# Performance work log

Measured on AMD Instinct MI355X. Metric: run time of the kernel, lower is better.

The kernel has to match this reference:

```python
import jax, jax.numpy as jnp
import numpy as np

B, T, NLAT, N, D = 8, 4, 64, 2048, 1024
HEADS, HEAD_DIM = 16, 64
ADIM = HEADS * HEAD_DIM
EPS = 1e-5


def layer_norm(x, w, b):
    mu = jnp.mean(x, axis=-1, keepdims=True)
    var = jnp.var(x, axis=-1, keepdims=True)
    return (x - mu) * jax.lax.rsqrt(var + EPS) * w + b


def setup_inputs() -> dict:
    key = jax.random.key(0)
    ks = jax.random.split(key, 8)
    s = 0.02
    return {
        "latents": jax.random.normal(ks[0], (B, T, NLAT, D), jnp.float32),
        "x": jax.random.normal(ks[1], (B, T, N, D), jnp.float32),
        "Wq": jax.random.normal(ks[2], (D, ADIM), jnp.float32) * s,     # [in, out]
        "Wkv": jax.random.normal(ks[3], (D, 2 * ADIM), jnp.float32) * s,
        "Wout": jax.random.normal(ks[4], (ADIM, D), jnp.float32) * s,
        "bout": jnp.zeros((D,), jnp.float32),
        "lnl_w": jnp.ones((D,), jnp.float32),
        "lnl_b": jnp.zeros((D,), jnp.float32),
        "lnm_w": jnp.ones((D,), jnp.float32),
        "lnm_b": jnp.zeros((D,), jnp.float32),
    }


def reference(latents, x, Wq, Wkv, Wout, bout, lnl_w, lnl_b, lnm_w, lnm_b):
    scale = HEAD_DIM ** (-0.5)
    lat = layer_norm(latents, lnl_w, lnl_b)          # [B,T,NLAT,D]
    med = layer_norm(x, lnm_w, lnm_b)                # [B,T,N,D]
    q = lat @ Wq                                      # [B,T,NLAT,ADIM]
    kv_in = jnp.concatenate((med, lat), axis=-2)      # [B,T,N+NLAT,D]
    kv = kv_in @ Wkv                                  # [B,T,N+NLAT,2*ADIM]
    k, v = jnp.split(kv, 2, axis=-1)
    # split heads: b t n (h d) -> b h t n d
    def split_heads(z):
        b, t, n, _ = z.shape
        return z.reshape(b, t, n, HEADS, HEAD_DIM).transpose(0, 3, 1, 2, 4)
    q = split_heads(q) * scale
    k = split_heads(k)
    v = split_heads(v)
    scores = jnp.einsum('bhtid,bhtjd->bhtij', q, k)   # [B,H,T,NLAT,N+NLAT]
    attn = jax.nn.softmax(scores, axis=-1)            # max-subtract handled internally
    out = jnp.einsum('bhtij,bhtjd->bhtid', attn, v)   # [B,H,T,NLAT,HEAD_DIM]
    out = out.transpose(0, 2, 3, 1, 4).reshape(B, T, NLAT, ADIM)
    return out @ Wout + bout
```

## Files before the change

kernel.cpp:

```cpp
#include <hip/hip_runtime.h>
#include <hip/hip_bf16.h>
#include <stdint.h>

#define B_    8
#define T_    4
#define NLAT  64
#define NMED  2048
#define NKV   2112
#define D_    1024
#define HEADS 16
#define HD    64
#define ADIM  1024
#define BT    32

#define GK    1024
#define GN    2048
#define GM    67584
#define NSLC  32
#define NWG_BIG 2144

typedef __attribute__((ext_vector_type(8))) short bf16x8;
typedef __attribute__((ext_vector_type(4))) float f32x4;

__device__ __forceinline__ ushort f2bf(float f) {
  union { float f; uint32_t u; } v; v.f = f;
  return (ushort)((v.u + 0x7fff + ((v.u >> 16) & 1)) >> 16);
}

__device__ __forceinline__ void gload_lds16(const void* g, void* l) {
  __builtin_amdgcn_global_load_lds(
      (const __attribute__((address_space(1))) void*)g,
      (__attribute__((address_space(3))) void*)l, 16, 0, 0);
}

__device__ __forceinline__ f32x4 mfma16(bf16x8 a, bf16x8 b, f32x4 c) {
  return __builtin_amdgcn_mfma_f32_16x16x32_bf16(a, b, c, 0, 0, 0);
}

__global__ __launch_bounds__(256) void wtrans(const float* __restrict__ src,
                                              ushort* __restrict__ dst,
                                              int K, int Nm) {
  __shared__ float t[64][65];
  const int tr = blockIdx.y, tc = blockIdx.x;
  const int c = threadIdx.x & 63;
  const int r4 = threadIdx.x >> 6;
#pragma unroll
  for (int rr = 0; rr < 16; ++rr) {
    int r = r4 + rr * 4;
    t[r][c] = src[(size_t)(tr * 64 + r) * Nm + tc * 64 + c];
  }
  __syncthreads();
#pragma unroll
  for (int rr = 0; rr < 16; ++rr) {
    int n = r4 + rr * 4;
    dst[(size_t)(tc * 64 + n) * K + tr * 64 + c] = f2bf(t[c][n]);
  }
}

__global__ __launch_bounds__(256) void ln_kernel(
    const float* __restrict__ lat, const float* __restrict__ x,
    const float* __restrict__ lnl_w, const float* __restrict__ lnl_b,
    const float* __restrict__ lnm_w, const float* __restrict__ lnm_b,
    ushort* __restrict__ kvin) {
  const int row = blockIdx.x;
  const int bt = row / NKV;
  const int j = row - bt * NKV;
  const float* src;
  const float* w;
  const float* bb;
  if (j < NMED) {
    src = x + ((size_t)bt * NMED + j) * D_;
    w = lnm_w; bb = lnm_b;
  } else {
    src = lat + ((size_t)bt * NLAT + (j - NMED)) * D_;
    w = lnl_w; bb = lnl_b;
  }
  const int tid = threadIdx.x;
  float4 v = ((const float4*)src)[tid];
  float s = v.x + v.y + v.z + v.w;
  float s2 = v.x * v.x + v.y * v.y + v.z * v.z + v.w * v.w;
#pragma unroll
  for (int off = 1; off < 64; off <<= 1) {
    s += __shfl_xor(s, off, 64);
    s2 += __shfl_xor(s2, off, 64);
  }
  __shared__ float red[8];
  const int wave = tid >> 6;
  if ((tid & 63) == 0) { red[wave] = s; red[4 + wave] = s2; }
  __syncthreads();
  float S = red[0] + red[1] + red[2] + red[3];
  float S2 = red[4] + red[5] + red[6] + red[7];
  const float inv = 1.f / (float)D_;
  float mu = S * inv;
  float var = S2 * inv - mu * mu;
  float rs = rsqrtf(var + 1e-5f);
  float4 wv = ((const float4*)w)[tid];
  float4 bv = ((const float4*)bb)[tid];
  ushort4 ov;
  ov.x = f2bf((v.x - mu) * rs * wv.x + bv.x);
  ov.y = f2bf((v.y - mu) * rs * wv.y + bv.y);
  ov.z = f2bf((v.z - mu) * rs * wv.z + bv.z);
  ov.w = f2bf((v.w - mu) * rs * wv.w + bv.w);
  ((ushort4*)(kvin + (size_t)row * D_))[tid] = ov;
}

template <int AMODE, int OUTMODE>
__global__ __launch_bounds__(256, 3) void gemm128(const ushort* __restrict__ A,
                                                  const ushort* __restrict__ Bt,
                                                  void* __restrict__ C,
                                                  const float* __restrict__ bias,
                                                  int ntx, int nwg, int K, int ldc) {
  __shared__ ushort lsA[128 * 32];
  __shared__ ushort lsB[128 * 32];
  const int tid = threadIdx.x;
  const int lane = tid & 63;
  const int wave = tid >> 6;
  const int lr = lane & 15;
  const int lg = lane >> 4;
  const int wr = (wave >> 1) * 64;
  const int wc = (wave & 1) * 64;

  const int g = blockIdx.x;
  const int cpx = nwg >> 3;
  const int v = (g & 7) * cpx + (g >> 3);
  const int bx = v % ntx;
  const int by = v / ntx;
  const long brow = (long)by * 128;
  const int bcol = bx * 128;

  const int pcx = lg ^ ((lr >> 1) & 3);

  f32x4 acc[4][4];
#pragma unroll
  for (int m = 0; m < 4; ++m)
#pragma unroll
    for (int n = 0; n < 4; ++n) acc[m][n] = (f32x4){0.f, 0.f, 0.f, 0.f};

  const int s0 = tid, s1 = 256 + tid;
  const int r0 = s0 >> 2, r1 = s1 >> 2;
  const int c0 = (s0 & 3) ^ ((s0 >> 3) & 3);
  const int c1 = (s1 & 3) ^ ((s1 >> 3) & 3);
  const int o0 = (s0 & ~63) * 16;
  const int o1 = (s1 & ~63) * 16;

  long arow0, arow1;
  if (AMODE == 1) {
    int g0 = (int)brow + r0, g1 = (int)brow + r1;
    arow0 = (long)(g0 >> 6) * NKV + NMED + (g0 & 63);
    arow1 = (long)(g1 >> 6) * NKV + NMED + (g1 & 63);
  } else {
    arow0 = brow + r0;
    arow1 = brow + r1;
  }
  const long browB0 = (long)(bcol + r0) * K;
  const long browB1 = (long)(bcol + r1) * K;

  for (int k0 = 0; k0 < K; k0 += 32) {
    gload_lds16(A + arow0 * (long)K + k0 + c0 * 8, (char*)lsA + o0);
    gload_lds16(A + arow1 * (long)K + k0 + c1 * 8, (char*)lsA + o1);
    gload_lds16(Bt + browB0 + k0 + c0 * 8, (char*)lsB + o0);
    gload_lds16(Bt + browB1 + k0 + c1 * 8, (char*)lsB + o1);
    __syncthreads();

    bf16x8 af[4], bf[4];
#pragma unroll
    for (int m = 0; m < 4; ++m)
      af[m] = *(const bf16x8*)((char*)lsA + (wr + m * 16 + lr) * 64 + pcx * 16);
#pragma unroll
    for (int n = 0; n < 4; ++n)
      bf[n] = *(const bf16x8*)((char*)lsB + (wc + n * 16 + lr) * 64 + pcx * 16);
#pragma unroll
    for (int m = 0; m < 4; ++m)
#pragma unroll
      for (int n = 0; n < 4; ++n)
        acc[m][n] = mfma16(bf[n], af[m], acc[m][n]);
    __syncthreads();
  }

#pragma unroll
  for (int m = 0; m < 4; ++m) {
    long row = brow + wr + m * 16 + lr;
#pragma unroll
    for (int n = 0; n < 4; ++n) {
      int coln = bcol + wc + n * 16 + lg * 4;
      long off = row * (long)ldc + coln;
      if (OUTMODE == 2) {
        float4 bv = *(const float4*)(bias + coln);
        float4 o;
        o.x = acc[m][n][0] + bv.x;
        o.y = acc[m][n][1] + bv.y;
        o.z = acc[m][n][2] + bv.z;
        o.w = acc[m][n][3] + bv.w;
        *(float4*)((float*)C + off) = o;
      } else {
        const float sc = (OUTMODE == 1) ? 0.125f : 1.f;
        ushort4 o;
        o.x = f2bf(acc[m][n][0] * sc);
        o.y = f2bf(acc[m][n][1] * sc);
        o.z = f2bf(acc[m][n][2] * sc);
        o.w = f2bf(acc[m][n][3] * sc);
        *(ushort4*)((ushort*)C + off) = o;
      }
    }
  }
}

__global__ __launch_bounds__(512, 2) void gemm256(const ushort* __restrict__ A,
                                                  const ushort* __restrict__ BtKV,
                                                  const ushort* __restrict__ BtQ,
                                                  ushort* __restrict__ Ckv,
                                                  ushort* __restrict__ Cq) {
  extern __shared__ __align__(16) char smem[];
  const int tid = threadIdx.x;
  const int lane = tid & 63;
  const int wv = tid >> 6;
  const int wm = wv >> 2;
  const int wn = wv & 3;
  const int lr = lane & 15;
  const int lg = lane >> 4;

  const int g = blockIdx.x;
  const int v = (g & 7) * (NWG_BIG / 8) + (g >> 3);
  const bool isq = v >= 2112;
  long brow; int bcol;
  const ushort* Bp; ushort* Cp; int ldc;
  if (!isq) {
    brow = (long)(v >> 3) * 256;
    bcol = (v & 7) * 256;
    Bp = BtKV; Cp = Ckv; ldc = GN;
  } else {
    int u = v - 2112;
    brow = (long)(u >> 2) * 256;
    bcol = (u & 3) * 256;
    Bp = BtQ; Cp = Cq; ldc = ADIM;
  }
  const float sc = isq ? 0.125f : 1.f;

  const int pcx = lg ^ ((lr >> 1) & 3);
  const int rbA = wm * 128 + lr;
  const int rbB = wn * 64 + lr;

  f32x4 acc[8][4];
#pragma unroll
  for (int m = 0; m < 8; ++m)
#pragma unroll
    for (int n = 0; n < 4; ++n) acc[m][n] = (f32x4){0.f, 0.f, 0.f, 0.f};

  const int s0 = tid, s1 = 512 + tid;
  const int r0 = s0 >> 2, r1 = s1 >> 2;
  const int c0 = (s0 & 3) ^ ((s0 >> 3) & 3);
  const int c1 = (s1 & 3) ^ ((s1 >> 3) & 3);
  const int o0 = (s0 & ~63) * 16;
  const int o1 = (s1 & ~63) * 16;

  long arow0, arow1;
  if (isq) {
    int g0 = (int)brow + r0, g1 = (int)brow + r1;
    arow0 = (long)(g0 >> 6) * NKV + NMED + (g0 & 63);
    arow1 = (long)(g1 >> 6) * NKV + NMED + (g1 & 63);
  } else {
    arow0 = brow + r0;
    arow1 = brow + r1;
  }

#define STAGE_A(slc, slot)                                                     \
  {                                                                            \
    long k0 = (long)(slc) * 32;                                                \
    char* db = smem + (slot) * 32768;                                          \
    gload_lds16(A + arow0 * (long)GK + k0 + c0 * 8, db + o0);                  \
    gload_lds16(A + arow1 * (long)GK + k0 + c1 * 8, db + o1);                  \
  }
#define STAGE_B(slc, slot)                                                     \
  {                                                                            \
    long k0 = (long)(slc) * 32;                                                \
    char* db = smem + (slot) * 32768 + 16384;                                  \
    gload_lds16(Bp + (long)(bcol + r0) * GK + k0 + c0 * 8, db + o0);           \
    gload_lds16(Bp + (long)(bcol + r1) * GK + k0 + c1 * 8, db + o1);           \
  }

  bf16x8 a0[4], a1[4], b0[4], b1[4];

  STAGE_A(0, 0); STAGE_B(0, 0);
  STAGE_A(1, 1); STAGE_B(1, 1);
  STAGE_A(2, 2); STAGE_B(2, 2);
  asm volatile("s_waitcnt vmcnt(8)" ::: "memory");
  __builtin_amdgcn_s_barrier();
#pragma unroll
  for (int m = 0; m < 4; ++m)
    a0[m] = *(const bf16x8*)(smem + (rbA + m * 16) * 64 + pcx * 16);
#pragma unroll
  for (int n = 0; n < 4; ++n)
    b0[n] = *(const bf16x8*)(smem + 16384 + (rbB + n * 16) * 64 + pcx * 16);
  __builtin_amdgcn_sched_barrier(0);

#define SLICE(T, BCUR, BNXT)                                                   \
  {                                                                            \
    const int t_ = (T);                                                        \
    const char* sA_ = smem + (t_ & 3) * 32768;                                 \
    const int ts_ = (t_ + 3 < NSLC) ? t_ + 3 : t_;                             \
    const int ws_ = (t_ + 3) & 3;                                              \
                                                        \
    _Pragma("unroll")                                                          \
    for (int m = 0; m < 4; ++m)                                                \
      a1[m] = *(const bf16x8*)(sA_ + (rbA + (m + 4) * 16) * 64 + pcx * 16);    \
    STAGE_A(ts_, ws_);                                                         \
    __builtin_amdgcn_sched_barrier(0);                                         \
    __builtin_amdgcn_s_barrier();                                              \
    asm volatile("s_waitcnt lgkmcnt(4)" ::: "memory");                         \
    __builtin_amdgcn_sched_barrier(0);                                         \
    __builtin_amdgcn_s_setprio(1);                                             \
    _Pragma("unroll")                                                          \
    for (int m = 0; m < 4; ++m)                                                \
      _Pragma("unroll")                                                        \
      for (int n = 0; n < 4; ++n)                                              \
        acc[m][n] = mfma16(BCUR[n], a0[m], acc[m][n]);                         \
    __builtin_amdgcn_s_setprio(0);                                             \
    __builtin_amdgcn_sched_barrier(0);                                         \
    __builtin_amdgcn_s_barrier();                                              \
                                                        \
    STAGE_B(ts_, ws_);                                                         \
    asm volatile("s_waitcnt vmcnt(8)" ::: "memory");                           \
    __builtin_amdgcn_sched_barrier(0);                                         \
    __builtin_amdgcn_s_barrier();                                              \
    {                                                                          \
      const int tn_ = (t_ + 1 < NSLC) ? t_ + 1 : t_;                           \
      const char* nA_ = smem + (tn_ & 3) * 32768;                              \
      const char* nB_ = nA_ + 16384;                                           \
      _Pragma("unroll")                                                        \
      for (int m = 0; m < 4; ++m)                                              \
        a0[m] = *(const bf16x8*)(nA_ + (rbA + m * 16) * 64 + pcx * 16);        \
      _Pragma("unroll")                                                        \
      for (int n = 0; n < 4; ++n)                                              \
        BNXT[n] = *(const bf16x8*)(nB_ + (rbB + n * 16) * 64 + pcx * 16);      \
    }                                                                          \
    __builtin_amdgcn_sched_barrier(0);                                         \
    asm volatile("s_waitcnt lgkmcnt(8)" ::: "memory");                         \
    __builtin_amdgcn_sched_barrier(0);                                         \
    __builtin_amdgcn_s_setprio(1);                                             \
    _Pragma("unroll")                                                          \
    for (int m = 0; m < 4; ++m)                                                \
      _Pragma("unroll")                                                        \
      for (int n = 0; n < 4; ++n)                                              \
        acc[m + 4][n] = mfma16(BCUR[n], a1[m], acc[m + 4][n]);                 \
    __builtin_amdgcn_s_setprio(0);                                             \
    __builtin_amdgcn_sched_barrier(0);                                         \
    __builtin_amdgcn_s_barrier();                                              \
  }

  for (int t = 0; t < NSLC; t += 2) {
    SLICE(t, b0, b1);
    SLICE(t + 1, b1, b0);
  }
#undef SLICE
#undef STAGE_A
#undef STAGE_B

#pragma unroll
  for (int m = 0; m < 8; ++m) {
    long row = brow + wm * 128 + m * 16 + lr;
    ushort* crow = Cp + row * ldc + bcol + wn * 64 + lg * 4;
#pragma unroll
    for (int n = 0; n < 4; ++n) {
      ushort4 o;
      o.x = f2bf(acc[m][n][0] * sc);
      o.y = f2bf(acc[m][n][1] * sc);
      o.z = f2bf(acc[m][n][2] * sc);
      o.w = f2bf(acc[m][n][3] * sc);
      *(ushort4*)(crow + n * 16) = o;
    }
  }
}

__global__ __launch_bounds__(256) void attn_kernel(const ushort* __restrict__ q,
                                                   const ushort* __restrict__ kv,
                                                   ushort* __restrict__ o) {
  const int blk = blockIdx.x;
  const int bt = blk >> 4;
  const int h = blk & 15;
  const int tid = threadIdx.x;
  const int wave = tid >> 6;
  const int lane = tid & 63;
  const int lr = lane & 15;
  const int lg = lane >> 4;

  __shared__ ushort klb[2][64 * 64];
  __shared__ ushort vtb[2][64 * 72];
  __shared__ ushort pl[4][16][72];

  const ushort* qbase = q + (size_t)(bt * 64 + wave * 16) * ADIM + h * HD;
  bf16x8 qf[2];
#pragma unroll
  for (int ks = 0; ks < 2; ++ks)
    qf[ks] = *(const bf16x8*)(qbase + (size_t)lr * ADIM + ks * 32 + lg * 8);

  const ushort* kvb = kv + (size_t)bt * NKV * 2048;
  const int jj = tid >> 2;
  const int q4 = tid & 3;

  f32x4 accO[4];
#pragma unroll
  for (int n = 0; n < 4; ++n) accO[n] = (f32x4){0.f, 0.f, 0.f, 0.f};
  float mrun = -1e30f;
  float lrun = 0.f;

  bf16x8 kr0, kr1, vr0, vr1;
  {
    const ushort* src = kvb + (size_t)jj * 2048 + h * HD + q4 * 16;
    kr0 = *(const bf16x8*)(src);
    kr1 = *(const bf16x8*)(src + 8);
    vr0 = *(const bf16x8*)(src + ADIM);
    vr1 = *(const bf16x8*)(src + ADIM + 8);
  }

  for (int jt = 0; jt < NKV / 64; ++jt) {
    const int pb = jt & 1;
    ushort* kl = klb[pb];
    ushort* vtf = vtb[pb];

    {
      int p0 = (q4 * 2) ^ (jj & 7);
      int p1 = (q4 * 2 + 1) ^ (jj & 7);
      *(bf16x8*)((char*)kl + jj * 128 + p0 * 16) = kr0;
      *(bf16x8*)((char*)kl + jj * 128 + p1 * 16) = kr1;
      int d0 = q4 * 16;
      int jc = jj >> 3, jb = jj & 7;
#pragma unroll
      for (int e = 0; e < 8; ++e) {
        vtf[(d0 + e) * 72 + (jc ^ (e & 7)) * 8 + jb] = ((const ushort*)&vr0)[e];
        vtf[(d0 + 8 + e) * 72 + (jc ^ (e & 7)) * 8 + jb] = ((const ushort*)&vr1)[e];
      }
    }

    bf16x8 nk0, nk1, nv0, nv1;
    {
      const int tn = (jt + 1 < NKV / 64) ? jt + 1 : jt;
      const ushort* src = kvb + (size_t)(tn * 64 + jj) * 2048 + h * HD + q4 * 16;
      nk0 = *(const bf16x8*)(src);
      nk1 = *(const bf16x8*)(src + 8);
      nv0 = *(const bf16x8*)(src + ADIM);
      nv1 = *(const bf16x8*)(src + ADIM + 8);
    }
    __syncthreads();

    f32x4 s[4];
#pragma unroll
    for (int nj = 0; nj < 4; ++nj) s[nj] = (f32x4){0.f, 0.f, 0.f, 0.f};
    __builtin_amdgcn_s_setprio(1);
#pragma unroll
    for (int nj = 0; nj < 4; ++nj)
#pragma unroll
      for (int ks = 0; ks < 2; ++ks) {
        int row = nj * 16 + lr;
        int phys = (4 * ks + lg) ^ (lr & 7);
        bf16x8 kf = *(const bf16x8*)((char*)kl + row * 128 + phys * 16);
        s[nj] = mfma16(kf, qf[ks], s[nj]);
      }
    __builtin_amdgcn_s_setprio(0);

    float mloc = s[0][0];
#pragma unroll
    for (int nj = 0; nj < 4; ++nj)
#pragma unroll
      for (int r = 0; r < 4; ++r) mloc = fmaxf(mloc, s[nj][r]);
    mloc = fmaxf(mloc, __shfl_xor(mloc, 16, 64));
    mloc = fmaxf(mloc, __shfl_xor(mloc, 32, 64));
    float mn = fmaxf(mrun, mloc);
    float corr = __expf(mrun - mn);
    mrun = mn;
    float ps = 0.f;
#pragma unroll
    for (int nj = 0; nj < 4; ++nj)
#pragma unroll
      for (int r = 0; r < 4; ++r) {
        float pv = __expf(s[nj][r] - mn);
        s[nj][r] = pv;
        ps += pv;
      }
    ps += __shfl_xor(ps, 16, 64);
    ps += __shfl_xor(ps, 32, 64);
    lrun = lrun * corr + ps;
    float corrq[4];
#pragma unroll
    for (int r = 0; r < 4; ++r) corrq[r] = __shfl(corr, lg * 4 + r, 64);
#pragma unroll
    for (int n = 0; n < 4; ++n)
#pragma unroll
      for (int r = 0; r < 4; ++r) accO[n][r] *= corrq[r];

#pragma unroll
    for (int nj = 0; nj < 4; ++nj)
#pragma unroll
      for (int r = 0; r < 4; ++r)
        pl[wave][lr][nj * 16 + 4 * lg + r] = f2bf(s[nj][r]);

    bf16x8 pf[2];
#pragma unroll
    for (int ks = 0; ks < 2; ++ks)
      pf[ks] = *(const bf16x8*)&pl[wave][lr][ks * 32 + lg * 8];
    __builtin_amdgcn_s_setprio(1);
#pragma unroll
    for (int nd = 0; nd < 4; ++nd)
#pragma unroll
      for (int ks = 0; ks < 2; ++ks) {
        bf16x8 vf = *(const bf16x8*)&vtf[(nd * 16 + lr) * 72 +
                                         ((4 * ks + lg) ^ (lr & 7)) * 8];
        accO[nd] = mfma16(pf[ks], vf, accO[nd]);
      }
    __builtin_amdgcn_s_setprio(0);

    kr0 = nk0; kr1 = nk1; vr0 = nv0; vr1 = nv1;
  }

  float lq[4];
#pragma unroll
  for (int r = 0; r < 4; ++r) lq[r] = __shfl(lrun, lg * 4 + r, 64);
#pragma unroll
  for (int nd = 0; nd < 4; ++nd)
#pragma unroll
    for (int r = 0; r < 4; ++r) {
      float vv = accO[nd][r] / lq[r];
      int row = bt * 64 + wave * 16 + lg * 4 + r;
      o[(size_t)row * ADIM + h * HD + nd * 16 + lr] = f2bf(vv);
    }
}

extern "C" void kernel_launch(void* const* d_in, const int* in_sizes, int n_in,
                              void* d_out, int out_size, void* d_ws, size_t ws_size,
                              hipStream_t stream) {
  const float* latents = (const float*)d_in[0];
  const float* x = (const float*)d_in[1];
  const float* Wq = (const float*)d_in[2];
  const float* Wkv = (const float*)d_in[3];
  const float* Wout = (const float*)d_in[4];
  const float* bout = (const float*)d_in[5];
  const float* lnl_w = (const float*)d_in[6];
  const float* lnl_b = (const float*)d_in[7];
  const float* lnm_w = (const float*)d_in[8];
  const float* lnm_b = (const float*)d_in[9];

  char* ws = (char*)d_ws;
  size_t off = 0;
  auto alloc = [&](size_t bytes) -> void* {
    void* p = ws + off;
    off += (bytes + 255) & ~(size_t)255;
    return p;
  };
  ushort* kvin = (ushort*)alloc((size_t)BT * NKV * D_ * 2);
  ushort* kvo  = (ushort*)alloc((size_t)BT * NKV * 2048 * 2);
  ushort* qb   = (ushort*)alloc((size_t)BT * NLAT * ADIM * 2);
  ushort* ao   = (ushort*)alloc((size_t)BT * NLAT * ADIM * 2);
  ushort* WqT  = (ushort*)alloc((size_t)D_ * ADIM * 2);
  ushort* WkvT = (ushort*)alloc((size_t)D_ * 2 * ADIM * 2);
  ushort* WoutT = (ushort*)alloc((size_t)ADIM * D_ * 2);

  hipFuncSetAttribute((const void*)gemm256,
                      hipFuncAttributeMaxDynamicSharedMemorySize, 131072);

  wtrans<<<dim3(ADIM / 64, D_ / 64), 256, 0, stream>>>(Wq, WqT, D_, ADIM);
  wtrans<<<dim3(2 * ADIM / 64, D_ / 64), 256, 0, stream>>>(Wkv, WkvT, D_, 2 * ADIM);
  wtrans<<<dim3(D_ / 64, ADIM / 64), 256, 0, stream>>>(Wout, WoutT, ADIM, D_);

  ln_kernel<<<BT * NKV, 256, 0, stream>>>(latents, x, lnl_w, lnl_b, lnm_w, lnm_b, kvin);

  gemm256<<<dim3(NWG_BIG), 512, 131072, stream>>>(kvin, WkvT, WqT, kvo, qb);

  attn_kernel<<<BT * HEADS, 256, 0, stream>>>(qb, kvo, ao);

  gemm128<0, 2><<<dim3(128), 256, 0, stream>>>(
      ao, WoutT, d_out, bout, D_ / 128, 128, ADIM, D_);
}
```

Measured before the change: 515.2 us.

## Shrink big GEMM tile to 128x256, merge weight transposes, wave-per-row layernorm

```diff
diff --git a/kernel.cpp b/kernel.cpp
--- a/kernel.cpp
+++ b/kernel.cpp
@@ -17,7 +17,7 @@
 #define GN    2048
 #define GM    67584
 #define NSLC  32
-#define NWG_BIG 2144
+#define NWGB  4288
 
 typedef __attribute__((ext_vector_type(8))) short bf16x8;
 typedef __attribute__((ext_vector_type(4))) float f32x4;
@@ -37,11 +37,20 @@
   return __builtin_amdgcn_mfma_f32_16x16x32_bf16(a, b, c, 0, 0, 0);
 }
 
-__global__ __launch_bounds__(256) void wtrans(const float* __restrict__ src,
-                                              ushort* __restrict__ dst,
-                                              int K, int Nm) {
+__global__ __launch_bounds__(256) void wtrans_all(
+    const float* __restrict__ Wq, const float* __restrict__ Wkv,
+    const float* __restrict__ Wout, ushort* __restrict__ WqT,
+    ushort* __restrict__ WkvT, ushort* __restrict__ WoutT) {
   __shared__ float t[64][65];
-  const int tr = blockIdx.y, tc = blockIdx.x;
+  int b = blockIdx.x;
+  const float* src; ushort* dst; int K, Nm, tr, tc;
+  if (b < 256) {
+    src = Wq; dst = WqT; K = 1024; Nm = 1024; tr = b >> 4; tc = b & 15;
+  } else if (b < 768) {
+    b -= 256; src = Wkv; dst = WkvT; K = 1024; Nm = 2048; tr = b >> 5; tc = b & 31;
+  } else {
+    b -= 768; src = Wout; dst = WoutT; K = 1024; Nm = 1024; tr = b >> 4; tc = b & 15;
+  }
   const int c = threadIdx.x & 63;
   const int r4 = threadIdx.x >> 6;
 #pragma unroll
@@ -62,7 +71,9 @@
     const float* __restrict__ lnl_w, const float* __restrict__ lnl_b,
     const float* __restrict__ lnm_w, const float* __restrict__ lnm_b,
     ushort* __restrict__ kvin) {
-  const int row = blockIdx.x;
+  const int wave = threadIdx.x >> 6;
+  const int lane = threadIdx.x & 63;
+  const int row = blockIdx.x * 4 + wave;
   const int bt = row / NKV;
   const int j = row - bt * NKV;
   const float* src;
@@ -75,142 +86,43 @@
     src = lat + ((size_t)bt * NLAT + (j - NMED)) * D_;
     w = lnl_w; bb = lnl_b;
   }
-  const int tid = threadIdx.x;
-  float4 v = ((const float4*)src)[tid];
-  float s = v.x + v.y + v.z + v.w;
-  float s2 = v.x * v.x + v.y * v.y + v.z * v.z + v.w * v.w;
+  float4 v[4];
+  float s = 0.f, s2 = 0.f;
+#pragma unroll
+  for (int c = 0; c < 4; ++c) {
+    v[c] = ((const float4*)src)[c * 64 + lane];
+    s += v[c].x + v[c].y + v[c].z + v[c].w;
+    s2 += v[c].x * v[c].x + v[c].y * v[c].y + v[c].z * v[c].z + v[c].w * v[c].w;
+  }
 #pragma unroll
   for (int off = 1; off < 64; off <<= 1) {
     s += __shfl_xor(s, off, 64);
     s2 += __shfl_xor(s2, off, 64);
   }
-  __shared__ float red[8];
-  const int wave = tid >> 6;
-  if ((tid & 63) == 0) { red[wave] = s; red[4 + wave] = s2; }
-  __syncthreads();
-  float S = red[0] + red[1] + red[2] + red[3];
-  float S2 = red[4] + red[5] + red[6] + red[7];
   const float inv = 1.f / (float)D_;
-  float mu = S * inv;
-  float var = S2 * inv - mu * mu;
+  float mu = s * inv;
+  float var = s2 * inv - mu * mu;
   float rs = rsqrtf(var + 1e-5f);
-  float4 wv = ((const float4*)w)[tid];
-  float4 bv = ((const float4*)bb)[tid];
-  ushort4 ov;
-  ov.x = f2bf((v.x - mu) * rs * wv.x + bv.x);
-  ov.y = f2bf((v.y - mu) * rs * wv.y + bv.y);
-  ov.z = f2bf((v.z - mu) * rs * wv.z + bv.z);
-  ov.w = f2bf((v.w - mu) * rs * wv.w + bv.w);
-  ((ushort4*)(kvin + (size_t)row * D_))[tid] = ov;
-}
-
-template <int AMODE, int OUTMODE>
-__global__ __launch_bounds__(256, 3) void gemm128(const ushort* __restrict__ A,
-                                                  const ushort* __restrict__ Bt,
-                                                  void* __restrict__ C,
-                                                  const float* __restrict__ bias,
-                                                  int ntx, int nwg, int K, int ldc) {
-  __shared__ ushort lsA[128 * 32];
-  __shared__ ushort lsB[128 * 32];
-  const int tid = threadIdx.x;
-  const int lane = tid & 63;
-  const int wave = tid >> 6;
-  const int lr = lane & 15;
-  const int lg = lane >> 4;
-  const int wr = (wave >> 1) * 64;
-  const int wc = (wave & 1) * 64;
-
-  const int g = blockIdx.x;
-  const int cpx = nwg >> 3;
-  const int v = (g & 7) * cpx + (g >> 3);
-  const int bx = v % ntx;
-  const int by = v / ntx;
-  const long brow = (long)by * 128;
-  const int bcol = bx * 128;
-
-  const int pcx = lg ^ ((lr >> 1) & 3);
-
-  f32x4 acc[4][4];
-#pragma unroll
-  for (int m = 0; m < 4; ++m)
-#pragma unroll
-    for (int n = 0; n < 4; ++n) acc[m][n] = (f32x4){0.f, 0.f, 0.f, 0.f};
-
-  const int s0 = tid, s1 = 256 + tid;
-  const int r0 = s0 >> 2, r1 = s1 >> 2;
-  const int c0 = (s0 & 3) ^ ((s0 >> 3) & 3);
-  const int c1 = (s1 & 3) ^ ((s1 >> 3) & 3);
-  const int o0 = (s0 & ~63) * 16;
-  const int o1 = (s1 & ~63) * 16;
-
-  long arow0, arow1;
-  if (AMODE == 1) {
-    int g0 = (int)brow + r0, g1 = (int)brow + r1;
-    arow0 = (long)(g0 >> 6) * NKV + NMED + (g0 & 63);
-    arow1 = (long)(g1 >> 6) * NKV + NMED + (g1 & 63);
-  } else {
-    arow0 = brow + r0;
-    arow1 = brow + r1;
-  }
-  const long browB0 = (long)(bcol + r0) * K;
-  const long browB1 = (long)(bcol + r1) * K;
-
-  for (int k0 = 0; k0 < K; k0 += 32) {
-    gload_lds16(A + arow0 * (long)K + k0 + c0 * 8, (char*)lsA + o0);
-    gload_lds16(A + arow1 * (long)K + k0 + c1 * 8, (char*)lsA + o1);
-    gload_lds16(Bt + browB0 + k0 + c0 * 8, (char*)lsB + o0);
-    gload_lds16(Bt + browB1 + k0 + c1 * 8, (char*)lsB + o1);
-    __syncthreads();
-
-    bf16x8 af[4], bf[4];
-#pragma unroll
-    for (int m = 0; m < 4; ++m)
-      af[m] = *(const bf16x8*)((char*)lsA + (wr + m * 16 + lr) * 64 + pcx * 16);
-#pragma unroll
-    for (int n = 0; n < 4; ++n)
-      bf[n] = *(const bf16x8*)((char*)lsB + (wc + n * 16 + lr) * 64 + pcx * 16);
-#pragma unroll
-    for (int m = 0; m < 4; ++m)
-#pragma unroll
-      for (int n = 0; n < 4; ++n)
-        acc[m][n] = mfma16(bf[n], af[m], acc[m][n]);
-    __syncthreads();
-  }
-
-#pragma unroll
-  for (int m = 0; m < 4; ++m) {
-    long row = brow + wr + m * 16 + lr;
-#pragma unroll
-    for (int n = 0; n < 4; ++n) {
-      int coln = bcol + wc + n * 16 + lg * 4;
-      long off = row * (long)ldc + coln;
-      if (OUTMODE == 2) {
-        float4 bv = *(const float4*)(bias + coln);
-        float4 o;
-        o.x = acc[m][n][0] + bv.x;
-        o.y = acc[m][n][1] + bv.y;
-        o.z = acc[m][n][2] + bv.z;
-        o.w = acc[m][n][3] + bv.w;
-        *(float4*)((float*)C + off) = o;
-      } else {
-        const float sc = (OUTMODE == 1) ? 0.125f : 1.f;
-        ushort4 o;
-        o.x = f2bf(acc[m][n][0] * sc);
-        o.y = f2bf(acc[m][n][1] * sc);
-        o.z = f2bf(acc[m][n][2] * sc);
-        o.w = f2bf(acc[m][n][3] * sc);
-        *(ushort4*)((ushort*)C + off) = o;
-      }
-    }
-  }
-}
-
-__global__ __launch_bounds__(512, 2) void gemm256(const ushort* __restrict__ A,
-                                                  const ushort* __restrict__ BtKV,
-                                                  const ushort* __restrict__ BtQ,
-                                                  ushort* __restrict__ Ckv,
-                                                  ushort* __restrict__ Cq) {
-  extern __shared__ __align__(16) char smem[];
+  ushort* dst = kvin + (size_t)row * D_;
+#pragma unroll
+  for (int c = 0; c < 4; ++c) {
+    float4 wv = ((const float4*)w)[c * 64 + lane];
+    float4 bv = ((const float4*)bb)[c * 64 + lane];
+    ushort4 ov;
+    ov.x = f2bf((v[c].x - mu) * rs * wv.x + bv.x);
+    ov.y = f2bf((v[c].y - mu) * rs * wv.y + bv.y);
+    ov.z = f2bf((v[c].z - mu) * rs * wv.z + bv.z);
+    ov.w = f2bf((v[c].w - mu) * rs * wv.w + bv.w);
+    ((ushort4*)dst)[c * 64 + lane] = ov;
+  }
+}
+
+__global__ __launch_bounds__(512, 4) void gemm_big(const ushort* __restrict__ A,
+                                                   const ushort* __restrict__ BtKV,
+                                                   const ushort* __restrict__ BtQ,
+                                                   ushort* __restrict__ Ckv,
+                                                   ushort* __restrict__ Cq) {
+  __shared__ __align__(16) char smem[2 * 24576];
   const int tid = threadIdx.x;
   const int lane = tid & 63;
   const int wv = tid >> 6;
@@ -220,144 +132,92 @@
   const int lg = lane >> 4;
 
   const int g = blockIdx.x;
-  const int v = (g & 7) * (NWG_BIG / 8) + (g >> 3);
-  const bool isq = v >= 2112;
+  const int v = (g & 7) * (NWGB / 8) + (g >> 3);
+  const bool isq = v >= 4224;
   long brow; int bcol;
   const ushort* Bp; ushort* Cp; int ldc;
   if (!isq) {
-    brow = (long)(v >> 3) * 256;
+    brow = (long)(v >> 3) * 128;
     bcol = (v & 7) * 256;
     Bp = BtKV; Cp = Ckv; ldc = GN;
   } else {
-    int u = v - 2112;
-    brow = (long)(u >> 2) * 256;
+    int u = v - 4224;
+    brow = (long)(u >> 2) * 128;
     bcol = (u & 3) * 256;
     Bp = BtQ; Cp = Cq; ldc = ADIM;
   }
   const float sc = isq ? 0.125f : 1.f;
 
   const int pcx = lg ^ ((lr >> 1) & 3);
-  const int rbA = wm * 128 + lr;
-  const int rbB = wn * 64 + lr;
-
-  f32x4 acc[8][4];
-#pragma unroll
-  for (int m = 0; m < 8; ++m)
+
+  f32x4 acc[4][4];
+#pragma unroll
+  for (int m = 0; m < 4; ++m)
 #pragma unroll
     for (int n = 0; n < 4; ++n) acc[m][n] = (f32x4){0.f, 0.f, 0.f, 0.f};
 
-  const int s0 = tid, s1 = 512 + tid;
-  const int r0 = s0 >> 2, r1 = s1 >> 2;
-  const int c0 = (s0 & 3) ^ ((s0 >> 3) & 3);
-  const int c1 = (s1 & 3) ^ ((s1 >> 3) & 3);
-  const int o0 = (s0 & ~63) * 16;
-  const int o1 = (s1 & ~63) * 16;
-
-  long arow0, arow1;
+  const int rA = tid >> 2;
+  const int lc = (tid & 3) ^ ((tid >> 3) & 3);
+  const int offA = (tid & ~63) * 16;
+  const int rB1 = 128 + (tid >> 2);
+  const int offB1 = 8192 + offA;
+
+  long arow;
   if (isq) {
-    int g0 = (int)brow + r0, g1 = (int)brow + r1;
-    arow0 = (long)(g0 >> 6) * NKV + NMED + (g0 & 63);
-    arow1 = (long)(g1 >> 6) * NKV + NMED + (g1 & 63);
+    int g0 = (int)brow + rA;
+    arow = (long)(g0 >> 6) * NKV + NMED + (g0 & 63);
   } else {
-    arow0 = brow + r0;
-    arow1 = brow + r1;
-  }
-
-#define STAGE_A(slc, slot)                                                     \
+    arow = brow + rA;
+  }
+
+#define STAGE(buf, kt)                                                         \
   {                                                                            \
-    long k0 = (long)(slc) * 32;                                                \
-    char* db = smem + (slot) * 32768;                                          \
-    gload_lds16(A + arow0 * (long)GK + k0 + c0 * 8, db + o0);                  \
-    gload_lds16(A + arow1 * (long)GK + k0 + c1 * 8, db + o1);                  \
-  }
-#define STAGE_B(slc, slot)                                                     \
-  {                                                                            \
-    long k0 = (long)(slc) * 32;                                                \
-    char* db = smem + (slot) * 32768 + 16384;                                  \
-    gload_lds16(Bp + (long)(bcol + r0) * GK + k0 + c0 * 8, db + o0);           \
-    gload_lds16(Bp + (long)(bcol + r1) * GK + k0 + c1 * 8, db + o1);           \
-  }
-
-  bf16x8 a0[4], a1[4], b0[4], b1[4];
-
-  STAGE_A(0, 0); STAGE_B(0, 0);
-  STAGE_A(1, 1); STAGE_B(1, 1);
-  STAGE_A(2, 2); STAGE_B(2, 2);
-  asm volatile("s_waitcnt vmcnt(8)" ::: "memory");
-  __builtin_amdgcn_s_barrier();
-#pragma unroll
-  for (int m = 0; m < 4; ++m)
-    a0[m] = *(const bf16x8*)(smem + (rbA + m * 16) * 64 + pcx * 16);
-#pragma unroll
-  for (int n = 0; n < 4; ++n)
-    b0[n] = *(const bf16x8*)(smem + 16384 + (rbB + n * 16) * 64 + pcx * 16);
-  __builtin_amdgcn_sched_barrier(0);
-
-#define SLICE(T, BCUR, BNXT)                                                   \
-  {                                                                            \
-    const int t_ = (T);                                                        \
-    const char* sA_ = smem + (t_ & 3) * 32768;                                 \
-    const int ts_ = (t_ + 3 < NSLC) ? t_ + 3 : t_;                             \
-    const int ws_ = (t_ + 3) & 3;                                              \
-                                                        \
-    _Pragma("unroll")                                                          \
-    for (int m = 0; m < 4; ++m)                                                \
-      a1[m] = *(const bf16x8*)(sA_ + (rbA + (m + 4) * 16) * 64 + pcx * 16);    \
-    STAGE_A(ts_, ws_);                                                         \
-    __builtin_amdgcn_sched_barrier(0);                                         \
-    __builtin_amdgcn_s_barrier();                                              \
-    asm volatile("s_waitcnt lgkmcnt(4)" ::: "memory");                         \
-    __builtin_amdgcn_sched_barrier(0);                                         \
-    __builtin_amdgcn_s_setprio(1);                                             \
-    _Pragma("unroll")                                                          \
-    for (int m = 0; m < 4; ++m)                                                \
-      _Pragma("unroll")                                                        \
-      for (int n = 0; n < 4; ++n)                                              \
-        acc[m][n] = mfma16(BCUR[n], a0[m], acc[m][n]);                         \
-    __builtin_amdgcn_s_setprio(0);                                             \
-    __builtin_amdgcn_sched_barrier(0);                                         \
-    __builtin_amdgcn_s_barrier();                                              \
-                                                        \
-    STAGE_B(ts_, ws_);                                                         \
-    asm volatile("s_waitcnt vmcnt(8)" ::: "memory");                           \
-    __builtin_amdgcn_sched_barrier(0);                                         \
-    __builtin_amdgcn_s_barrier();                                              \
-    {                                                                          \
-      const int tn_ = (t_ + 1 < NSLC) ? t_ + 1 : t_;                           \
-      const char* nA_ = smem + (tn_ & 3) * 32768;                              \
-      const char* nB_ = nA_ + 16384;                                           \
-      _Pragma("unroll")                                                        \
-      for (int m = 0; m < 4; ++m)                                              \
-        a0[m] = *(const bf16x8*)(nA_ + (rbA + m * 16) * 64 + pcx * 16);        \
-      _Pragma("unroll")                                                        \
-      for (int n = 0; n < 4; ++n)                                              \
-        BNXT[n] = *(const bf16x8*)(nB_ + (rbB + n * 16) * 64 + pcx * 16);      \
-    }                                                                          \
-    __builtin_amdgcn_sched_barrier(0);                                         \
-    asm volatile("s_waitcnt lgkmcnt(8)" ::: "memory");                         \
-    __builtin_amdgcn_sched_barrier(0);                                         \
-    __builtin_amdgcn_s_setprio(1);                                             \
-    _Pragma("unroll")                                                          \
-    for (int m = 0; m < 4; ++m)                                                \
-      _Pragma("unroll")                                                        \
-      for (int n = 0; n < 4; ++n)                                              \
-        acc[m + 4][n] = mfma16(BCUR[n], a1[m], acc[m + 4][n]);                 \
-    __builtin_amdgcn_s_setprio(0);                                             \
-    __builtin_amdgcn_sched_barrier(0);                                         \
-    __builtin_amdgcn_s_barrier();                                              \
-  }
-
-  for (int t = 0; t < NSLC; t += 2) {
-    SLICE(t, b0, b1);
-    SLICE(t + 1, b1, b0);
-  }
-#undef SLICE
-#undef STAGE_A
-#undef STAGE_B
-
-#pragma unroll
-  for (int m = 0; m < 8; ++m) {
-    long row = brow + wm * 128 + m * 16 + lr;
+    long k0 = (long)(kt) * 32;                                                 \
+    char* dbA = smem + (buf) * 24576;                                          \
+    char* dbB = dbA + 8192;                                                    \
+    gload_lds16(A + arow * (long)GK + k0 + lc * 8, dbA + offA);                \
+    gload_lds16(Bp + (long)(bcol + rA) * GK + k0 + lc * 8, dbB + offA);        \
+    gload_lds16(Bp + (long)(bcol + rB1) * GK + k0 + lc * 8, dbB + offB1);      \
+  }
+
+  STAGE(0, 0);
+
+  for (int t = 0; t < NSLC; ++t) {
+    const int p = t & 1;
+    __builtin_amdgcn_s_barrier();
+    asm volatile("" ::: "memory");
+    const int ts = (t + 1 < NSLC) ? t + 1 : t;
+    STAGE(p ^ 1, ts);
+    asm volatile("s_waitcnt vmcnt(3)" ::: "memory");
+    __builtin_amdgcn_s_barrier();
+    asm volatile("" ::: "memory");
+
+    const char* bufA = smem + p * 24576;
+    const char* bufB = bufA + 8192;
+    bf16x8 af[4], bf[4];
+#pragma unroll
+    for (int m = 0; m < 4; ++m) {
+      int row = wm * 64 + m * 16 + lr;
+      af[m] = *(const bf16x8*)(bufA + row * 64 + pcx * 16);
+    }
+#pragma unroll
+    for (int n = 0; n < 4; ++n) {
+      int row = wn * 64 + n * 16 + lr;
+      bf[n] = *(const bf16x8*)(bufB + row * 64 + pcx * 16);
+    }
+    __builtin_amdgcn_s_setprio(1);
+#pragma unroll
+    for (int m = 0; m < 4; ++m)
+#pragma unroll
+      for (int n = 0; n < 4; ++n)
+        acc[m][n] = mfma16(bf[n], af[m], acc[m][n]);
+    __builtin_amdgcn_s_setprio(0);
+  }
+#undef STAGE
+
+#pragma unroll
+  for (int m = 0; m < 4; ++m) {
+    long row = brow + wm * 64 + m * 16 + lr;
     ushort* crow = Cp + row * ldc + bcol + wn * 64 + lg * 4;
 #pragma unroll
     for (int n = 0; n < 4; ++n) {
@@ -367,6 +227,79 @@
       o.z = f2bf(acc[m][n][2] * sc);
       o.w = f2bf(acc[m][n][3] * sc);
       *(ushort4*)(crow + n * 16) = o;
+    }
+  }
+}
+
+__global__ __launch_bounds__(256, 3) void gemm_out(const ushort* __restrict__ A,
+                                                   const ushort* __restrict__ Bt,
+                                                   float* __restrict__ C,
+                                                   const float* __restrict__ bias) {
+  __shared__ ushort lsA[64 * 32];
+  __shared__ ushort lsB[128 * 32];
+  const int tid = threadIdx.x;
+  const int lane = tid & 63;
+  const int wave = tid >> 6;
+  const int lr = lane & 15;
+  const int lg = lane >> 4;
+  const int wr = (wave >> 1) * 32;
+  const int wc = (wave & 1) * 64;
+
+  const int g = blockIdx.x;
+  const int v = (g & 7) * 32 + (g >> 3);
+  const int bx = v & 7;
+  const int by = v >> 3;
+  const long brow = (long)by * 64;
+  const int bcol = bx * 128;
+
+  const int pcx = lg ^ ((lr >> 1) & 3);
+
+  f32x4 acc[2][4];
+#pragma unroll
+  for (int m = 0; m < 2; ++m)
+#pragma unroll
+    for (int n = 0; n < 4; ++n) acc[m][n] = (f32x4){0.f, 0.f, 0.f, 0.f};
+
+  const int rA = tid >> 2;
+  const int lc = (tid & 3) ^ ((tid >> 3) & 3);
+  const int offA = (tid & ~63) * 16;
+  const int rB1 = 64 + (tid >> 2);
+  const int offB1 = 4096 + offA;
+
+  for (int k0 = 0; k0 < ADIM; k0 += 32) {
+    gload_lds16(A + (brow + rA) * (long)ADIM + k0 + lc * 8, (char*)lsA + offA);
+    gload_lds16(Bt + (long)(bcol + rA) * ADIM + k0 + lc * 8, (char*)lsB + offA);
+    gload_lds16(Bt + (long)(bcol + rB1) * ADIM + k0 + lc * 8, (char*)lsB + offB1);
+    __syncthreads();
+
+    bf16x8 af[2], bf[4];
+#pragma unroll
+    for (int m = 0; m < 2; ++m)
+      af[m] = *(const bf16x8*)((char*)lsA + (wr + m * 16 + lr) * 64 + pcx * 16);
+#pragma unroll
+    for (int n = 0; n < 4; ++n)
+      bf[n] = *(const bf16x8*)((char*)lsB + (wc + n * 16 + lr) * 64 + pcx * 16);
+#pragma unroll
+    for (int m = 0; m < 2; ++m)
+#pragma unroll
+      for (int n = 0; n < 4; ++n)
+        acc[m][n] = mfma16(bf[n], af[m], acc[m][n]);
+    __syncthreads();
+  }
+
+#pragma unroll
+  for (int m = 0; m < 2; ++m) {
+    long row = brow + wr + m * 16 + lr;
+#pragma unroll
+    for (int n = 0; n < 4; ++n) {
+      int coln = bcol + wc + n * 16 + lg * 4;
+      float4 bv = *(const float4*)(bias + coln);
+      float4 o;
+      o.x = acc[m][n][0] + bv.x;
+      o.y = acc[m][n][1] + bv.y;
+      o.z = acc[m][n][2] + bv.z;
+      o.w = acc[m][n][3] + bv.w;
+      *(float4*)(C + row * (long)D_ + coln) = o;
     }
   }
 }
@@ -553,19 +486,13 @@
   ushort* WkvT = (ushort*)alloc((size_t)D_ * 2 * ADIM * 2);
   ushort* WoutT = (ushort*)alloc((size_t)ADIM * D_ * 2);
 
-  hipFuncSetAttribute((const void*)gemm256,
-                      hipFuncAttributeMaxDynamicSharedMemorySize, 131072);
-
-  wtrans<<<dim3(ADIM / 64, D_ / 64), 256, 0, stream>>>(Wq, WqT, D_, ADIM);
-  wtrans<<<dim3(2 * ADIM / 64, D_ / 64), 256, 0, stream>>>(Wkv, WkvT, D_, 2 * ADIM);
-  wtrans<<<dim3(D_ / 64, ADIM / 64), 256, 0, stream>>>(Wout, WoutT, ADIM, D_);
-
-  ln_kernel<<<BT * NKV, 256, 0, stream>>>(latents, x, lnl_w, lnl_b, lnm_w, lnm_b, kvin);
-
-  gemm256<<<dim3(NWG_BIG), 512, 131072, stream>>>(kvin, WkvT, WqT, kvo, qb);
+  wtrans_all<<<dim3(1024), 256, 0, stream>>>(Wq, Wkv, Wout, WqT, WkvT, WoutT);
+
+  ln_kernel<<<GM / 4, 256, 0, stream>>>(latents, x, lnl_w, lnl_b, lnm_w, lnm_b, kvin);
+
+  gemm_big<<<dim3(NWGB), 512, 0, stream>>>(kvin, WkvT, WqT, kvo, qb);
 
   attn_kernel<<<BT * HEADS, 256, 0, stream>>>(qb, kvo, ao);
 
-  gemm128<0, 2><<<dim3(128), 256, 0, stream>>>(
-      ao, WoutT, d_out, bout, D_ / 128, 128, ADIM, D_);
-}
+  gemm_out<<<dim3(256), 256, 0, stream>>>(ao, WoutT, (float*)d_out, bout);
+}
```

New measurement: 495.5 us. 3.8% less time.
